# Optimization experiments

Hardware: AMD Instinct MI355X
Metric: run time of the kernel (lower is better)

Reference implementation:

```python
import jax, jax.numpy as jnp
import numpy as np

C = 64          # channels / d_model
D_INNER = 128   # expand * C
D_STATE = 16
D_CONV = 4
DT_RANK = 4     # ceil(C / 16)
GROUPS = 4
EPS = 1e-5


def setup_inputs() -> dict:
    key = jax.random.key(0)
    ks = jax.random.split(key, 12)
    b, h, w = 2, 128, 128
    s = 0.02
    return {
        "x": jax.random.normal(ks[0], (b, C, h, w), jnp.float32),
        "in_proj_w": jax.random.normal(ks[1], (2 * D_INNER, C), jnp.float32) * s,
        "conv_w": jax.random.normal(ks[2], (D_INNER, D_CONV), jnp.float32) * s,
        "conv_b": jnp.zeros((D_INNER,), jnp.float32),
        "x_proj_w": jax.random.normal(ks[3], (DT_RANK + 2 * D_STATE, D_INNER), jnp.float32) * s,
        "dt_proj_w": jax.random.normal(ks[4], (D_INNER, DT_RANK), jnp.float32) * s,
        "dt_proj_b": jax.random.normal(ks[5], (D_INNER,), jnp.float32) * s,
        "A_log": jnp.log(jnp.broadcast_to(jnp.arange(1, D_STATE + 1, dtype=jnp.float32), (D_INNER, D_STATE))),
        "D": jnp.ones((D_INNER,), jnp.float32),
        "out_proj_w": jax.random.normal(ks[6], (C, D_INNER), jnp.float32) * s,
        "gn_scale": jnp.ones((C,), jnp.float32),
        "gn_bias": jnp.zeros((C,), jnp.float32),
    }


def _mamba(xr, in_proj_w, conv_w, conv_b, x_proj_w, dt_proj_w, dt_proj_b, A_log, D, out_proj_w):
    # xr: (b, L, C)
    b, L, _ = xr.shape
    xz = jnp.einsum('blc,ec->ble', xr, in_proj_w)          # (b, L, 2*d_inner)
    xc, z = jnp.split(xz, 2, axis=-1)
    # causal depthwise conv1d, kernel D_CONV
    xp = jnp.pad(xc, ((0, 0), (D_CONV - 1, 0), (0, 0)))
    xconv = sum(conv_w[:, k] * xp[:, k:k + L, :] for k in range(D_CONV)) + conv_b
    u = jax.nn.silu(xconv)                                  # (b, L, d_inner)
    dbc = jnp.einsum('bld,ed->ble', u, x_proj_w)
    dt_r = dbc[..., :DT_RANK]
    Bm = dbc[..., DT_RANK:DT_RANK + D_STATE]                # (b, L, d_state)
    Cm = dbc[..., DT_RANK + D_STATE:]                       # (b, L, d_state)
    dt = jax.nn.softplus(jnp.einsum('blr,dr->bld', dt_r, dt_proj_w) + dt_proj_b)
    A = -jnp.exp(A_log)                                     # (d_inner, d_state)
    deltaA = jnp.exp(dt[..., None] * A)                     # (b, L, d_inner, d_state)
    deltaBu = (dt * u)[..., None] * Bm[:, :, None, :]       # (b, L, d_inner, d_state)

    def step(hst, inp):
        dA_t, dBu_t, C_t = inp
        hst = dA_t * hst + dBu_t                            # (b, d_inner, d_state)
        y_t = jnp.einsum('bds,bs->bd', hst, C_t)
        return hst, y_t

    h0 = jnp.zeros((b, D_INNER, D_STATE), xr.dtype)
    _, ys = jax.lax.scan(step, h0, (jnp.moveaxis(deltaA, 1, 0), jnp.moveaxis(deltaBu, 1, 0), jnp.moveaxis(Cm, 1, 0)))
    y = jnp.moveaxis(ys, 0, 1) + u * D                      # (b, L, d_inner)
    y = y * jax.nn.silu(z)
    return jnp.einsum('bld,cd->blc', y, out_proj_w)


def _group_norm_silu(x, scale, bias):
    # x: (b, C, h, w)
    b, c, h, w = x.shape
    xg = x.reshape(b, GROUPS, c // GROUPS, h, w)
    mu = xg.mean(axis=(2, 3, 4), keepdims=True)
    var = xg.var(axis=(2, 3, 4), keepdims=True)
    xn = ((xg - mu) * jax.lax.rsqrt(var + EPS)).reshape(b, c, h, w)
    return jax.nn.silu(xn * scale[None, :, None, None] + bias[None, :, None, None])


def reference(x, in_proj_w, conv_w, conv_b, x_proj_w, dt_proj_w, dt_proj_b, A_log, D, out_proj_w, gn_scale, gn_bias):
    b, c, h, w = x.shape
    xr = jnp.transpose(x, (0, 2, 3, 1)).reshape(b, h * w, c)
    y = _mamba(xr, in_proj_w, conv_w, conv_b, x_proj_w, dt_proj_w, dt_proj_b, A_log, D, out_proj_w)
    y = jnp.transpose(y.reshape(b, h, w, c), (0, 3, 1, 2))
    y = _group_norm_silu(y, gn_scale, gn_bias)
    return y + x
```

## Files before the change

kernel.cpp:

```cpp
#include <hip/hip_runtime.h>

#define BB 2
#define CCH 64
#define LLEN 16384
#define DM 128
#define NCHK 512
#define TCHK 32
#define NGRP 32
#define JG 16
#define NG 4

#define OFF_XC   0ull
#define OFF_HEND 0ull
#define OFF_HLOC 2097152ull
#define OFF_Z    4194304ull
#define OFF_U    8388608ull
#define OFF_DT   12582912ull
#define OFF_BM   16777216ull
#define OFF_CM   17301504ull
#define OFF_DTS  17825792ull
#define OFF_YM   17956864ull
#define OFF_WC   17956864ull
#define OFF_STAT 20054016ull
#define OFF_CUMDT 20971520ull
#define OFF_GEND  21102592ull
#define OFF_GDT   21233664ull
#define OFF_GINIT 21241856ull

__device__ __forceinline__ float fsilu(float v) {
  return v * __builtin_amdgcn_rcpf(1.f + __expf(-v));
}
__device__ __forceinline__ float fsoftplus(float v) {
  return v > 20.f ? v : __logf(1.f + __expf(v));
}

__global__ __launch_bounds__(256) void k1_inproj(
    const float* __restrict__ x, const float* __restrict__ w,
    float* __restrict__ xc, float* __restrict__ z)
{
  const int b = blockIdx.z;
  const int l0 = blockIdx.x * 64;
  const int e0 = blockIdx.y * 64;
  __shared__ float As[64][68];
  __shared__ float Bs[64][68];
  const int t = threadIdx.x;
#pragma unroll
  for (int i = 0; i < 4; i++) {
    int f4 = t + i * 256;
    int c = f4 >> 4, tok4 = (f4 & 15) * 4;
    *reinterpret_cast<float4*>(&As[c][tok4]) =
        *reinterpret_cast<const float4*>(&x[(size_t)(b * CCH + c) * LLEN + l0 + tok4]);
  }
#pragma unroll
  for (int i = 0; i < 16; i++) {
    int idx = t + i * 256;
    int e = idx >> 6, c = idx & 63;
    Bs[c][e] = w[(e0 + e) * CCH + c];
  }
  __syncthreads();
  const int tm = (t & 15) * 4;
  const int tn = (t >> 4) * 4;
  float acc[4][4] = {};
  for (int c = 0; c < 64; c++) {
    float4 av = *reinterpret_cast<const float4*>(&As[c][tm]);
    float4 bv = *reinterpret_cast<const float4*>(&Bs[c][tn]);
    acc[0][0] += av.x * bv.x; acc[0][1] += av.x * bv.y; acc[0][2] += av.x * bv.z; acc[0][3] += av.x * bv.w;
    acc[1][0] += av.y * bv.x; acc[1][1] += av.y * bv.y; acc[1][2] += av.y * bv.z; acc[1][3] += av.y * bv.w;
    acc[2][0] += av.z * bv.x; acc[2][1] += av.z * bv.y; acc[2][2] += av.z * bv.z; acc[2][3] += av.z * bv.w;
    acc[3][0] += av.w * bv.x; acc[3][1] += av.w * bv.y; acc[3][2] += av.w * bv.z; acc[3][3] += av.w * bv.w;
  }
  float* dst = (e0 < DM) ? (xc + e0) : (z + (e0 - DM));
#pragma unroll
  for (int i = 0; i < 4; i++) {
    int l = l0 + tm + i;
    float4 v = make_float4(acc[i][0], acc[i][1], acc[i][2], acc[i][3]);
    *reinterpret_cast<float4*>(dst + (size_t)(b * LLEN + l) * DM + tn) = v;
  }
}

__global__ __launch_bounds__(256) void k0_wcomb(
    const float* __restrict__ xpw, const float* __restrict__ dtw, float* __restrict__ wc,
    float* __restrict__ stat)
{
  int i = blockIdx.x * 256 + threadIdx.x;
  if (blockIdx.x == 0 && threadIdx.x < BB * NG * 2) stat[threadIdx.x] = 0.f;
  if (i >= 160 * 128) return;
  int e = i >> 7, dd = i & 127;
  float v;
  if (e < 128) {
    v = dtw[e * 4 + 0] * xpw[0 * 128 + dd] + dtw[e * 4 + 1] * xpw[1 * 128 + dd]
      + dtw[e * 4 + 2] * xpw[2 * 128 + dd] + dtw[e * 4 + 3] * xpw[3 * 128 + dd];
  } else {
    v = xpw[(e - 128 + 4) * 128 + dd];
  }
  wc[i] = v;
}

__global__ __launch_bounds__(256) void k2a_conv(
    const float* __restrict__ xc, const float* __restrict__ cw, const float* __restrict__ cb,
    float* __restrict__ u)
{
  const int t = threadIdx.x;
  const int d4 = (t & 31) * 4;
  const int tg = t >> 5;
  const int tok0 = blockIdx.x * 64 + tg * 8;
  const int l0 = tok0 & (LLEN - 1);
  float4 w0 = *reinterpret_cast<const float4*>(cw + (d4 + 0) * 4);
  float4 w1 = *reinterpret_cast<const float4*>(cw + (d4 + 1) * 4);
  float4 w2 = *reinterpret_cast<const float4*>(cw + (d4 + 2) * 4);
  float4 w3 = *reinterpret_cast<const float4*>(cw + (d4 + 3) * 4);
  float4 bias = *reinterpret_cast<const float4*>(cb + d4);
  float4 row[11];
#pragma unroll
  for (int r = 0; r < 11; r++) {
    int l = l0 - 3 + r;
    if (l < 0) row[r] = make_float4(0.f, 0.f, 0.f, 0.f);
    else row[r] = *reinterpret_cast<const float4*>(xc + (size_t)(tok0 - 3 + r) * DM + d4);
  }
#pragma unroll
  for (int j = 0; j < 8; j++) {
    float4 acc;
    acc.x = bias.x + w0.x * row[j].x + w0.y * row[j+1].x + w0.z * row[j+2].x + w0.w * row[j+3].x;
    acc.y = bias.y + w1.x * row[j].y + w1.y * row[j+1].y + w1.z * row[j+2].y + w1.w * row[j+3].y;
    acc.z = bias.z + w2.x * row[j].z + w2.y * row[j+1].z + w2.z * row[j+2].z + w2.w * row[j+3].z;
    acc.w = bias.w + w3.x * row[j].w + w3.y * row[j+1].w + w3.z * row[j+2].w + w3.w * row[j+3].w;
    acc.x = fsilu(acc.x); acc.y = fsilu(acc.y); acc.z = fsilu(acc.z); acc.w = fsilu(acc.w);
    *reinterpret_cast<float4*>(u + (size_t)(tok0 + j) * DM + d4) = acc;
  }
}

__global__ __launch_bounds__(128) void k2b_proj(
    const float* __restrict__ u, const float* __restrict__ wc, const float* __restrict__ dtpb,
    float* __restrict__ dt, float* __restrict__ bm, float* __restrict__ cm)
{
  const int tok0 = blockIdx.x * 64;
  const int e0 = blockIdx.y * 32;
  const int t = threadIdx.x;
  __shared__ float As[64][68];
  __shared__ float Bs[64][36];
  const int tm = (t & 15) * 4;
  const int tn = (t >> 4) * 4;
  float acc[4][4] = {};
  for (int kb = 0; kb < 2; kb++) {
#pragma unroll
    for (int i2 = 0; i2 < 2; i2++) {
      int tile = t + i2 * 128;
      int kt4 = (tile & 15) * 4, tok4 = (tile >> 4) * 4;
      const float* gp = u + (size_t)(tok0 + tok4) * DM + kb * 64 + kt4;
      float4 r0 = *reinterpret_cast<const float4*>(gp + 0 * DM);
      float4 r1 = *reinterpret_cast<const float4*>(gp + 1 * DM);
      float4 r2 = *reinterpret_cast<const float4*>(gp + 2 * DM);
      float4 r3 = *reinterpret_cast<const float4*>(gp + 3 * DM);
      *reinterpret_cast<float4*>(&As[kt4 + 0][tok4]) = make_float4(r0.x, r1.x, r2.x, r3.x);
      *reinterpret_cast<float4*>(&As[kt4 + 1][tok4]) = make_float4(r0.y, r1.y, r2.y, r3.y);
      *reinterpret_cast<float4*>(&As[kt4 + 2][tok4]) = make_float4(r0.z, r1.z, r2.z, r3.z);
      *reinterpret_cast<float4*>(&As[kt4 + 3][tok4]) = make_float4(r0.w, r1.w, r2.w, r3.w);
    }
    {
      int kt4 = (t & 15) * 4, et4 = (t >> 4) * 4;
      const float* gp = wc + (size_t)(e0 + et4) * DM + kb * 64 + kt4;
      float4 r0 = *reinterpret_cast<const float4*>(gp + 0 * DM);
      float4 r1 = *reinterpret_cast<const float4*>(gp + 1 * DM);
      float4 r2 = *reinterpret_cast<const float4*>(gp + 2 * DM);
      float4 r3 = *reinterpret_cast<const float4*>(gp + 3 * DM);
      *reinterpret_cast<float4*>(&Bs[kt4 + 0][et4]) = make_float4(r0.x, r1.x, r2.x, r3.x);
      *reinterpret_cast<float4*>(&Bs[kt4 + 1][et4]) = make_float4(r0.y, r1.y, r2.y, r3.y);
      *reinterpret_cast<float4*>(&Bs[kt4 + 2][et4]) = make_float4(r0.z, r1.z, r2.z, r3.z);
      *reinterpret_cast<float4*>(&Bs[kt4 + 3][et4]) = make_float4(r0.w, r1.w, r2.w, r3.w);
    }
    __syncthreads();
#pragma unroll 4
    for (int k = 0; k < 64; k++) {
      float4 av = *reinterpret_cast<const float4*>(&As[k][tm]);
      float4 bv = *reinterpret_cast<const float4*>(&Bs[k][tn]);
      acc[0][0] += av.x * bv.x; acc[0][1] += av.x * bv.y; acc[0][2] += av.x * bv.z; acc[0][3] += av.x * bv.w;
      acc[1][0] += av.y * bv.x; acc[1][1] += av.y * bv.y; acc[1][2] += av.y * bv.z; acc[1][3] += av.y * bv.w;
      acc[2][0] += av.z * bv.x; acc[2][1] += av.z * bv.y; acc[2][2] += av.z * bv.z; acc[2][3] += av.z * bv.w;
      acc[3][0] += av.w * bv.x; acc[3][1] += av.w * bv.y; acc[3][2] += av.w * bv.z; acc[3][3] += av.w * bv.w;
    }
    __syncthreads();
  }
  float* Cs = &As[0][0];
#pragma unroll
  for (int i = 0; i < 4; i++) {
#pragma unroll
    for (int j = 0; j < 4; j++) Cs[(tm + i) * 33 + tn + j] = acc[i][j];
  }
  __syncthreads();
  if (e0 < DM) {
#pragma unroll
    for (int i = 0; i < 16; i++) {
      int idx = t + i * 128;
      int tok = idx >> 5, e = idx & 31;
      float v = fsoftplus(Cs[tok * 33 + e] + dtpb[e0 + e]);
      dt[(size_t)(tok0 + tok) * DM + e0 + e] = v;
    }
  } else {
#pragma unroll
    for (int i = 0; i < 16; i++) {
      int idx = t + i * 128;
      int tok = idx >> 5, e = idx & 31;
      float v = Cs[tok * 33 + e];
      if (e < 16) bm[(size_t)(tok0 + tok) * 16 + e] = v;
      else        cm[(size_t)(tok0 + tok) * 16 + (e - 16)] = v;
    }
  }
}

__global__ __launch_bounds__(128) void k3_scan1(
    const float* __restrict__ dt, const float* __restrict__ u, const float* __restrict__ bm,
    const float* __restrict__ alog, float* __restrict__ hend, float* __restrict__ dts)
{
  const int b = blockIdx.y, ch = blockIdx.x;
  const int d = threadIdx.x;
  __shared__ float sb[TCHK][16];
  const size_t tok0 = (size_t)b * LLEN + (size_t)ch * TCHK;
  reinterpret_cast<float4*>(&sb[0][0])[d] = reinterpret_cast<const float4*>(bm + tok0 * 16)[d];
  float A[16];
  {
    const float4* ap = reinterpret_cast<const float4*>(alog + d * 16);
#pragma unroll
    for (int q = 0; q < 4; q++) {
      float4 v = ap[q];
      A[q * 4 + 0] = -__expf(v.x); A[q * 4 + 1] = -__expf(v.y);
      A[q * 4 + 2] = -__expf(v.z); A[q * 4 + 3] = -__expf(v.w);
    }
  }
  __syncthreads();
  float h[16];
#pragma unroll
  for (int s = 0; s < 16; s++) h[s] = 0.f;
  float dsum = 0.f;
  const float* dtp = dt + tok0 * DM + d;
  const float* up  = u  + tok0 * DM + d;
  for (int i = 0; i < TCHK; i++) {
    float dtv = dtp[(size_t)i * DM];
    float uv  = up[(size_t)i * DM];
    float dtu = dtv * uv;
    dsum += dtv;
    float bv[16];
#pragma unroll
    for (int q = 0; q < 4; q++)
      *reinterpret_cast<float4*>(&bv[q * 4]) = *reinterpret_cast<const float4*>(&sb[i][q * 4]);
#pragma unroll
    for (int s = 0; s < 16; s++) {
      float da = __expf(dtv * A[s]);
      h[s] = da * h[s] + dtu * bv[s];
    }
  }
  float* hp = hend + ((size_t)(b * DM + d) * NCHK + ch) * 16;
#pragma unroll
  for (int q = 0; q < 4; q++)
    reinterpret_cast<float4*>(hp)[q] = make_float4(h[q*4], h[q*4+1], h[q*4+2], h[q*4+3]);
  dts[(size_t)(b * DM + d) * NCHK + ch] = dsum;
}

__global__ __launch_bounds__(256) void k4a_group(
    const float* __restrict__ alog, const float* __restrict__ dts, const float* __restrict__ hend,
    float* __restrict__ hlocal, float* __restrict__ cumdt,
    float* __restrict__ gend, float* __restrict__ gdt)
{
  const int tid = blockIdx.x * 256 + threadIdx.x;
  const int s = tid & 15;
  const int bdg = tid >> 4;
  const int g = bdg & (NGRP - 1);
  const int bd = bdg >> 5;
  const int d = bd & (DM - 1);
  const float A = -__expf(alog[d * 16 + s]);
  const int ch0 = g * JG;
  const float* hp = hend + ((size_t)bd * NCHK + ch0) * 16 + s;
  const float* dp = dts + (size_t)bd * NCHK + ch0;
  float* hl = hlocal + ((size_t)bd * NCHK + ch0) * 16 + s;
  float hb[JG], db[JG];
#pragma unroll
  for (int j = 0; j < JG; j++) { hb[j] = hp[j * 16]; db[j] = dp[j]; }
  float h = 0.f, cd = 0.f;
#pragma unroll
  for (int j = 0; j < JG; j++) {
    hl[j * 16] = h;
    if (s == 0) cumdt[(size_t)(ch0 + j) * (BB * DM) + bd] = cd;
    h = __expf(A * db[j]) * h + hb[j];
    cd += db[j];
  }
  gend[(size_t)bdg * 16 + s] = h;
  if (s == 0) gdt[bdg] = cd;
}

__global__ __launch_bounds__(64) void k4b_combine(
    const float* __restrict__ alog, const float* __restrict__ gdt, const float* __restrict__ gend,
    float* __restrict__ ginit)
{
  const int tid = blockIdx.x * 64 + threadIdx.x;
  const int s = tid & 15, bd = tid >> 4, d = bd & (DM - 1);
  const float A = -__expf(alog[d * 16 + s]);
  const float* ge = gend + (size_t)bd * NGRP * 16 + s;
  const float* gd = gdt + (size_t)bd * NGRP;
  float* gi = ginit + (size_t)bd * NGRP * 16 + s;
  float gb[NGRP], db[NGRP];
#pragma unroll
  for (int g = 0; g < NGRP; g++) { gb[g] = ge[g * 16]; db[g] = gd[g]; }
  float h = 0.f;
#pragma unroll
  for (int g = 0; g < NGRP; g++) {
    gi[g * 16] = h;
    h = __expf(A * db[g]) * h + gb[g];
  }
}

__global__ __launch_bounds__(256) void k5f_scan_out(
    const float* __restrict__ dt, const float* __restrict__ u, const float* __restrict__ bm,
    const float* __restrict__ cm, const float* __restrict__ alog, const float* __restrict__ Dv,
    const float* __restrict__ z, const float* __restrict__ hlocal,
    const float* __restrict__ cumdt, const float* __restrict__ ginit,
    const float* __restrict__ ow, float* __restrict__ ym, float* __restrict__ stat)
{
  const int b = blockIdx.y, bx = blockIdx.x;
  const int t = threadIdx.x;
  const int ch2 = t >> 7;
  const int d = t & 127;
  const int ch = bx * 2 + ch2;
  __shared__ float sb[2][TCHK][16];
  __shared__ float sc[2][TCHK][16];
  __shared__ float Ys[DM][72];
  __shared__ float Bs[DM][68];
  const size_t tokb = (size_t)b * LLEN + (size_t)bx * 64;
  const size_t tok0 = tokb + (size_t)ch2 * TCHK;
  reinterpret_cast<float4*>(&sb[0][0][0])[t] = reinterpret_cast<const float4*>(bm + tokb * 16)[t];
  reinterpret_cast<float4*>(&sc[0][0][0])[t] = reinterpret_cast<const float4*>(cm + tokb * 16)[t];
#pragma unroll
  for (int i2 = 0; i2 < 2; i2++) {
    int tile = t + i2 * 256;
    int c4 = (tile & 15) * 4;
    int dl4 = (tile >> 4) * 4;
    const float* gp = ow + (size_t)c4 * DM + dl4;
    float4 r0 = *reinterpret_cast<const float4*>(gp + 0 * DM);
    float4 r1 = *reinterpret_cast<const float4*>(gp + 1 * DM);
    float4 r2 = *reinterpret_cast<const float4*>(gp + 2 * DM);
    float4 r3 = *reinterpret_cast<const float4*>(gp + 3 * DM);
    *reinterpret_cast<float4*>(&Bs[dl4 + 0][c4]) = make_float4(r0.x, r1.x, r2.x, r3.x);
    *reinterpret_cast<float4*>(&Bs[dl4 + 1][c4]) = make_float4(r0.y, r1.y, r2.y, r3.y);
    *reinterpret_cast<float4*>(&Bs[dl4 + 2][c4]) = make_float4(r0.z, r1.z, r2.z, r3.z);
    *reinterpret_cast<float4*>(&Bs[dl4 + 3][c4]) = make_float4(r0.w, r1.w, r2.w, r3.w);
  }
  float A[16];
  {
    const float4* ap = reinterpret_cast<const float4*>(alog + d * 16);
#pragma unroll
    for (int q = 0; q < 4; q++) {
      float4 v = ap[q];
      A[q * 4 + 0] = -__expf(v.x); A[q * 4 + 1] = -__expf(v.y);
      A[q * 4 + 2] = -__expf(v.z); A[q * 4 + 3] = -__expf(v.w);
    }
  }
  const float Dd = Dv[d];
  const int bd = b * DM + d;
  const int g = ch / JG;
  const float cd = cumdt[(size_t)ch * (BB * DM) + bd];
  float h[16];
  {
    const float4* hlp = reinterpret_cast<const float4*>(hlocal + ((size_t)bd * NCHK + ch) * 16);
    const float4* gip = reinterpret_cast<const float4*>(ginit + ((size_t)(bd * NGRP + g)) * 16);
#pragma unroll
    for (int q = 0; q < 4; q++) {
      float4 hl = hlp[q];
      float4 gi = gip[q];
      h[q * 4 + 0] = __expf(A[q * 4 + 0] * cd) * gi.x + hl.x;
      h[q * 4 + 1] = __expf(A[q * 4 + 1] * cd) * gi.y + hl.y;
      h[q * 4 + 2] = __expf(A[q * 4 + 2] * cd) * gi.z + hl.z;
      h[q * 4 + 3] = __expf(A[q * 4 + 3] * cd) * gi.w + hl.w;
    }
  }
  __syncthreads();
  const float* dtp = dt + tok0 * DM + d;
  const float* up = u + tok0 * DM + d;
  const float* zp = z + tok0 * DM + d;
  for (int i = 0; i < TCHK; i++) {
    float dtv = dtp[(size_t)i * DM];
    float uv  = up[(size_t)i * DM];
    float zv  = zp[(size_t)i * DM];
    float dtu = dtv * uv;
    float bv[16], cv[16];
#pragma unroll
    for (int q = 0; q < 4; q++) {
      *reinterpret_cast<float4*>(&bv[q * 4]) = *reinterpret_cast<const float4*>(&sb[ch2][i][q * 4]);
      *reinterpret_cast<float4*>(&cv[q * 4]) = *reinterpret_cast<const float4*>(&sc[ch2][i][q * 4]);
    }
    float y = 0.f;
#pragma unroll
    for (int s = 0; s < 16; s++) {
      float da = __expf(dtv * A[s]);
      h[s] = da * h[s] + dtu * bv[s];
      y += h[s] * cv[s];
    }
    Ys[d][ch2 * TCHK + i] = (y + uv * Dd) * fsilu(zv);
  }
  __syncthreads();
  const int tm = (t & 15) * 4;
  const int tn = (t >> 4) * 4;
  float acc[4][4] = {};
  for (int k = 0; k < DM; k++) {
    float4 av = *reinterpret_cast<const float4*>(&Ys[k][tm]);
    float4 bv = *reinterpret_cast<const float4*>(&Bs[k][tn]);
    acc[0][0] += av.x * bv.x; acc[0][1] += av.x * bv.y; acc[0][2] += av.x * bv.z; acc[0][3] += av.x * bv.w;
    acc[1][0] += av.y * bv.x; acc[1][1] += av.y * bv.y; acc[1][2] += av.y * bv.z; acc[1][3] += av.y * bv.w;
    acc[2][0] += av.z * bv.x; acc[2][1] += av.z * bv.y; acc[2][2] += av.z * bv.z; acc[2][3] += av.z * bv.w;
    acc[3][0] += av.w * bv.x; acc[3][1] += av.w * bv.y; acc[3][2] += av.w * bv.z; acc[3][3] += av.w * bv.w;
  }
  float lsum = 0.f, lssq = 0.f;
#pragma unroll
  for (int i = 0; i < 4; i++) {
    float4 v = make_float4(acc[i][0], acc[i][1], acc[i][2], acc[i][3]);
    *reinterpret_cast<float4*>(ym + (tokb + tm + i) * 64 + tn) = v;
    lsum += v.x + v.y + v.z + v.w;
    lssq += v.x * v.x + v.y * v.y + v.z * v.z + v.w * v.w;
  }
  __shared__ float sg[NG * 2];
  if (t < NG * 2) sg[t] = 0.f;
  __syncthreads();
  const int gg = tn >> 4;
  atomicAdd(&sg[gg * 2 + 0], lsum);
  atomicAdd(&sg[gg * 2 + 1], lssq);
  __syncthreads();
  if (t < NG * 2) atomicAdd(&stat[b * NG * 2 + t], sg[t]);
}

__global__ __launch_bounds__(256) void k7_gn(
    const float* __restrict__ ym, const float* __restrict__ stat,
    const float* __restrict__ scale, const float* __restrict__ bias,
    const float* __restrict__ x, float* __restrict__ out)
{
  const int b = blockIdx.y;
  const int p0 = blockIdx.x * 64;
  const int t = threadIdx.x;
  __shared__ float Ts[64][65];
#pragma unroll
  for (int i = 0; i < 16; i++) {
    int idx = t + i * 256;
    int p = idx >> 6, c = idx & 63;
    Ts[c][p] = ym[(size_t)(b * LLEN + p0 + p) * 64 + c];
  }
  __syncthreads();
  const float invN = 1.f / (16.f * 16384.f);
#pragma unroll
  for (int i = 0; i < 16; i++) {
    int idx = t + i * 256;
    int c = idx >> 6, p = idx & 63;
    int g = c >> 4;
    float mu = stat[b * 8 + g * 2] * invN;
    float var = stat[b * 8 + g * 2 + 1] * invN - mu * mu;
    float rs = rsqrtf(var + 1e-5f);
    float v = (Ts[c][p] - mu) * rs * scale[c] + bias[c];
    size_t o = (size_t)(b * CCH + c) * LLEN + p0 + p;
    out[o] = fsilu(v) + x[o];
  }
}

extern "C" void kernel_launch(void* const* d_in, const int* in_sizes, int n_in,
                              void* d_out, int out_size, void* d_ws, size_t ws_size,
                              hipStream_t stream)
{
  const float* x    = (const float*)d_in[0];
  const float* ipw  = (const float*)d_in[1];
  const float* cw   = (const float*)d_in[2];
  const float* cb   = (const float*)d_in[3];
  const float* xpw  = (const float*)d_in[4];
  const float* dtw  = (const float*)d_in[5];
  const float* dtpb = (const float*)d_in[6];
  const float* alog = (const float*)d_in[7];
  const float* Dv   = (const float*)d_in[8];
  const float* ow   = (const float*)d_in[9];
  const float* gns  = (const float*)d_in[10];
  const float* gnb  = (const float*)d_in[11];

  float* ws    = (float*)d_ws;
  float* xc    = ws + OFF_XC;
  float* hend  = ws + OFF_HEND;
  float* hloc  = ws + OFF_HLOC;
  float* z     = ws + OFF_Z;
  float* u     = ws + OFF_U;
  float* dt    = ws + OFF_DT;
  float* bm    = ws + OFF_BM;
  float* cm    = ws + OFF_CM;
  float* dts   = ws + OFF_DTS;
  float* ym    = ws + OFF_YM;
  float* wc    = ws + OFF_WC;
  float* cumdt = ws + OFF_CUMDT;
  float* gend  = ws + OFF_GEND;
  float* gdt   = ws + OFF_GDT;
  float* ginit = ws + OFF_GINIT;
  float* stat  = ws + OFF_STAT;
  float* out   = (float*)d_out;

  k0_wcomb<<<dim3(80), 256, 0, stream>>>(xpw, dtw, wc, stat);
  k1_inproj<<<dim3(LLEN / 64, 4, BB), 256, 0, stream>>>(x, ipw, xc, z);
  k2a_conv<<<dim3(BB * LLEN / 64), 256, 0, stream>>>(xc, cw, cb, u);
  k2b_proj<<<dim3(BB * LLEN / 64, 5), 128, 0, stream>>>(u, wc, dtpb, dt, bm, cm);
  k3_scan1<<<dim3(NCHK, BB), 128, 0, stream>>>(dt, u, bm, alog, hend, dts);
  k4a_group<<<dim3(BB * DM * NGRP * 16 / 256), 256, 0, stream>>>(alog, dts, hend, hloc, cumdt, gend, gdt);
  k4b_combine<<<dim3(BB * DM * 16 / 64), 64, 0, stream>>>(alog, gdt, gend, ginit);
  k5f_scan_out<<<dim3(NCHK / 2, BB), 256, 0, stream>>>(dt, u, bm, cm, alog, Dv, z, hloc, cumdt, ginit, ow, ym, stat);
  k7_gn<<<dim3(LLEN / 64, BB), 256, 0, stream>>>(ym, stat, gns, gnb, x, out);
}
```

Baseline: 133.4 us.

## Split scan state across thread pairs, fold weight-combine kernel into in-proj, use exp2

Both scan kernels now give each (channel, chunk) two threads that each hold half of the 16 SSM states. The output kernel combines their partial y with a lane shuffle and runs the out-projection with 512 threads on smaller tiles. This doubles the number of threads working on the latency-bound serial recurrences, and exponentials switch to exp2 with a log2e-prescaled A. The separate weight-combine/stat-zero kernel is merged into block (0,0,0) of the in-proj kernel to save a launch. That one block now does extra serial work, and the per-thread dt/u loads are duplicated across each thread pair.

```diff
diff --git a/kernel.cpp b/kernel.cpp
--- a/kernel.cpp
+++ b/kernel.cpp
@@ -9,6 +9,7 @@
 #define NGRP 32
 #define JG 16
 #define NG 4
+#define LOG2E 1.44269504f
 
 #define OFF_XC   0ull
 #define OFF_HEND 0ull
@@ -36,14 +37,30 @@
 
 __global__ __launch_bounds__(256) void k1_inproj(
     const float* __restrict__ x, const float* __restrict__ w,
-    float* __restrict__ xc, float* __restrict__ z)
+    float* __restrict__ xc, float* __restrict__ z,
+    const float* __restrict__ xpw, const float* __restrict__ dtw,
+    float* __restrict__ wc, float* __restrict__ stat)
 {
   const int b = blockIdx.z;
   const int l0 = blockIdx.x * 64;
   const int e0 = blockIdx.y * 64;
+  const int t = threadIdx.x;
+  if (blockIdx.x == 0 && blockIdx.y == 0 && blockIdx.z == 0) {
+    if (t < BB * NG * 2) stat[t] = 0.f;
+    for (int i = t; i < 160 * 128; i += 256) {
+      int e = i >> 7, dd = i & 127;
+      float v;
+      if (e < 128) {
+        v = dtw[e * 4 + 0] * xpw[0 * 128 + dd] + dtw[e * 4 + 1] * xpw[1 * 128 + dd]
+          + dtw[e * 4 + 2] * xpw[2 * 128 + dd] + dtw[e * 4 + 3] * xpw[3 * 128 + dd];
+      } else {
+        v = xpw[(e - 128 + 4) * 128 + dd];
+      }
+      wc[i] = v;
+    }
+  }
   __shared__ float As[64][68];
   __shared__ float Bs[64][68];
-  const int t = threadIdx.x;
 #pragma unroll
   for (int i = 0; i < 4; i++) {
     int f4 = t + i * 256;
@@ -76,24 +93,6 @@
     float4 v = make_float4(acc[i][0], acc[i][1], acc[i][2], acc[i][3]);
     *reinterpret_cast<float4*>(dst + (size_t)(b * LLEN + l) * DM + tn) = v;
   }
-}
-
-__global__ __launch_bounds__(256) void k0_wcomb(
-    const float* __restrict__ xpw, const float* __restrict__ dtw, float* __restrict__ wc,
-    float* __restrict__ stat)
-{
-  int i = blockIdx.x * 256 + threadIdx.x;
-  if (blockIdx.x == 0 && threadIdx.x < BB * NG * 2) stat[threadIdx.x] = 0.f;
-  if (i >= 160 * 128) return;
-  int e = i >> 7, dd = i & 127;
-  float v;
-  if (e < 128) {
-    v = dtw[e * 4 + 0] * xpw[0 * 128 + dd] + dtw[e * 4 + 1] * xpw[1 * 128 + dd]
-      + dtw[e * 4 + 2] * xpw[2 * 128 + dd] + dtw[e * 4 + 3] * xpw[3 * 128 + dd];
-  } else {
-    v = xpw[(e - 128 + 4) * 128 + dd];
-  }
-  wc[i] = v;
 }
 
 __global__ __launch_bounds__(256) void k2a_conv(
@@ -207,29 +206,32 @@
   }
 }
 
-__global__ __launch_bounds__(128) void k3_scan1(
+__global__ __launch_bounds__(256) void k3_scan1(
     const float* __restrict__ dt, const float* __restrict__ u, const float* __restrict__ bm,
     const float* __restrict__ alog, float* __restrict__ hend, float* __restrict__ dts)
 {
   const int b = blockIdx.y, ch = blockIdx.x;
-  const int d = threadIdx.x;
+  const int t = threadIdx.x;
+  const int sh = t & 1;
+  const int d = t >> 1;
   __shared__ float sb[TCHK][16];
   const size_t tok0 = (size_t)b * LLEN + (size_t)ch * TCHK;
-  reinterpret_cast<float4*>(&sb[0][0])[d] = reinterpret_cast<const float4*>(bm + tok0 * 16)[d];
-  float A[16];
+  if (t < 128)
+    reinterpret_cast<float4*>(&sb[0][0])[t] = reinterpret_cast<const float4*>(bm + tok0 * 16)[t];
+  float A2[8];
   {
-    const float4* ap = reinterpret_cast<const float4*>(alog + d * 16);
-#pragma unroll
-    for (int q = 0; q < 4; q++) {
+    const float4* ap = reinterpret_cast<const float4*>(alog + d * 16 + sh * 8);
+#pragma unroll
+    for (int q = 0; q < 2; q++) {
       float4 v = ap[q];
-      A[q * 4 + 0] = -__expf(v.x); A[q * 4 + 1] = -__expf(v.y);
-      A[q * 4 + 2] = -__expf(v.z); A[q * 4 + 3] = -__expf(v.w);
-    }
-  }
-  __syncthreads();
-  float h[16];
-#pragma unroll
-  for (int s = 0; s < 16; s++) h[s] = 0.f;
+      A2[q * 4 + 0] = -__expf(v.x) * LOG2E; A2[q * 4 + 1] = -__expf(v.y) * LOG2E;
+      A2[q * 4 + 2] = -__expf(v.z) * LOG2E; A2[q * 4 + 3] = -__expf(v.w) * LOG2E;
+    }
+  }
+  __syncthreads();
+  float h[8];
+#pragma unroll
+  for (int s = 0; s < 8; s++) h[s] = 0.f;
   float dsum = 0.f;
   const float* dtp = dt + tok0 * DM + d;
   const float* up  = u  + tok0 * DM + d;
@@ -238,21 +240,21 @@
     float uv  = up[(size_t)i * DM];
     float dtu = dtv * uv;
     dsum += dtv;
-    float bv[16];
-#pragma unroll
-    for (int q = 0; q < 4; q++)
-      *reinterpret_cast<float4*>(&bv[q * 4]) = *reinterpret_cast<const float4*>(&sb[i][q * 4]);
-#pragma unroll
-    for (int s = 0; s < 16; s++) {
-      float da = __expf(dtv * A[s]);
+    float bv[8];
+#pragma unroll
+    for (int q = 0; q < 2; q++)
+      *reinterpret_cast<float4*>(&bv[q * 4]) = *reinterpret_cast<const float4*>(&sb[i][sh * 8 + q * 4]);
+#pragma unroll
+    for (int s = 0; s < 8; s++) {
+      float da = exp2f(dtv * A2[s]);
       h[s] = da * h[s] + dtu * bv[s];
     }
   }
-  float* hp = hend + ((size_t)(b * DM + d) * NCHK + ch) * 16;
-#pragma unroll
-  for (int q = 0; q < 4; q++)
+  float* hp = hend + ((size_t)(b * DM + d) * NCHK + ch) * 16 + sh * 8;
+#pragma unroll
+  for (int q = 0; q < 2; q++)
     reinterpret_cast<float4*>(hp)[q] = make_float4(h[q*4], h[q*4+1], h[q*4+2], h[q*4+3]);
-  dts[(size_t)(b * DM + d) * NCHK + ch] = dsum;
+  if (sh == 0) dts[(size_t)(b * DM + d) * NCHK + ch] = dsum;
 }
 
 __global__ __launch_bounds__(256) void k4a_group(
@@ -307,7 +309,7 @@
   }
 }
 
-__global__ __launch_bounds__(256) void k5f_scan_out(
+__global__ __launch_bounds__(512) void k5f_scan_out(
     const float* __restrict__ dt, const float* __restrict__ u, const float* __restrict__ bm,
     const float* __restrict__ cm, const float* __restrict__ alog, const float* __restrict__ Dv,
     const float* __restrict__ z, const float* __restrict__ hlocal,
@@ -316,22 +318,23 @@
 {
   const int b = blockIdx.y, bx = blockIdx.x;
   const int t = threadIdx.x;
-  const int ch2 = t >> 7;
-  const int d = t & 127;
+  const int sh = t & 1;
+  const int d = (t >> 1) & 127;
+  const int ch2 = t >> 8;
   const int ch = bx * 2 + ch2;
   __shared__ float sb[2][TCHK][16];
   __shared__ float sc[2][TCHK][16];
-  __shared__ float Ys[DM][72];
+  __shared__ float Ys[DM][66];
   __shared__ float Bs[DM][68];
   const size_t tokb = (size_t)b * LLEN + (size_t)bx * 64;
   const size_t tok0 = tokb + (size_t)ch2 * TCHK;
-  reinterpret_cast<float4*>(&sb[0][0][0])[t] = reinterpret_cast<const float4*>(bm + tokb * 16)[t];
-  reinterpret_cast<float4*>(&sc[0][0][0])[t] = reinterpret_cast<const float4*>(cm + tokb * 16)[t];
-#pragma unroll
-  for (int i2 = 0; i2 < 2; i2++) {
-    int tile = t + i2 * 256;
-    int c4 = (tile & 15) * 4;
-    int dl4 = (tile >> 4) * 4;
+  if (t < 256) {
+    reinterpret_cast<float4*>(&sb[0][0][0])[t] = reinterpret_cast<const float4*>(bm + tokb * 16)[t];
+    reinterpret_cast<float4*>(&sc[0][0][0])[t] = reinterpret_cast<const float4*>(cm + tokb * 16)[t];
+  }
+  {
+    int c4 = (t & 15) * 4;
+    int dl4 = (t >> 4) * 4;
     const float* gp = ow + (size_t)c4 * DM + dl4;
     float4 r0 = *reinterpret_cast<const float4*>(gp + 0 * DM);
     float4 r1 = *reinterpret_cast<const float4*>(gp + 1 * DM);
@@ -342,32 +345,32 @@
     *reinterpret_cast<float4*>(&Bs[dl4 + 2][c4]) = make_float4(r0.z, r1.z, r2.z, r3.z);
     *reinterpret_cast<float4*>(&Bs[dl4 + 3][c4]) = make_float4(r0.w, r1.w, r2.w, r3.w);
   }
-  float A[16];
+  float A2[8];
   {
-    const float4* ap = reinterpret_cast<const float4*>(alog + d * 16);
-#pragma unroll
-    for (int q = 0; q < 4; q++) {
+    const float4* ap = reinterpret_cast<const float4*>(alog + d * 16 + sh * 8);
+#pragma unroll
+    for (int q = 0; q < 2; q++) {
       float4 v = ap[q];
-      A[q * 4 + 0] = -__expf(v.x); A[q * 4 + 1] = -__expf(v.y);
-      A[q * 4 + 2] = -__expf(v.z); A[q * 4 + 3] = -__expf(v.w);
+      A2[q * 4 + 0] = -__expf(v.x) * LOG2E; A2[q * 4 + 1] = -__expf(v.y) * LOG2E;
+      A2[q * 4 + 2] = -__expf(v.z) * LOG2E; A2[q * 4 + 3] = -__expf(v.w) * LOG2E;
     }
   }
   const float Dd = Dv[d];
   const int bd = b * DM + d;
   const int g = ch / JG;
   const float cd = cumdt[(size_t)ch * (BB * DM) + bd];
-  float h[16];
+  float h[8];
   {
-    const float4* hlp = reinterpret_cast<const float4*>(hlocal + ((size_t)bd * NCHK + ch) * 16);
-    const float4* gip = reinterpret_cast<const float4*>(ginit + ((size_t)(bd * NGRP + g)) * 16);
-#pragma unroll
-    for (int q = 0; q < 4; q++) {
+    const float4* hlp = reinterpret_cast<const float4*>(hlocal + ((size_t)bd * NCHK + ch) * 16 + sh * 8);
+    const float4* gip = reinterpret_cast<const float4*>(ginit + ((size_t)(bd * NGRP + g)) * 16 + sh * 8);
+#pragma unroll
+    for (int q = 0; q < 2; q++) {
       float4 hl = hlp[q];
       float4 gi = gip[q];
-      h[q * 4 + 0] = __expf(A[q * 4 + 0] * cd) * gi.x + hl.x;
-      h[q * 4 + 1] = __expf(A[q * 4 + 1] * cd) * gi.y + hl.y;
-      h[q * 4 + 2] = __expf(A[q * 4 + 2] * cd) * gi.z + hl.z;
-      h[q * 4 + 3] = __expf(A[q * 4 + 3] * cd) * gi.w + hl.w;
+      h[q * 4 + 0] = exp2f(A2[q * 4 + 0] * cd) * gi.x + hl.x;
+      h[q * 4 + 1] = exp2f(A2[q * 4 + 1] * cd) * gi.y + hl.y;
+      h[q * 4 + 2] = exp2f(A2[q * 4 + 2] * cd) * gi.z + hl.z;
+      h[q * 4 + 3] = exp2f(A2[q * 4 + 3] * cd) * gi.w + hl.w;
     }
   }
   __syncthreads();
@@ -379,45 +382,44 @@
     float uv  = up[(size_t)i * DM];
     float zv  = zp[(size_t)i * DM];
     float dtu = dtv * uv;
-    float bv[16], cv[16];
-#pragma unroll
-    for (int q = 0; q < 4; q++) {
-      *reinterpret_cast<float4*>(&bv[q * 4]) = *reinterpret_cast<const float4*>(&sb[ch2][i][q * 4]);
-      *reinterpret_cast<float4*>(&cv[q * 4]) = *reinterpret_cast<const float4*>(&sc[ch2][i][q * 4]);
+    float bv[8], cv[8];
+#pragma unroll
+    for (int q = 0; q < 2; q++) {
+      *reinterpret_cast<float4*>(&bv[q * 4]) = *reinterpret_cast<const float4*>(&sb[ch2][i][sh * 8 + q * 4]);
+      *reinterpret_cast<float4*>(&cv[q * 4]) = *reinterpret_cast<const float4*>(&sc[ch2][i][sh * 8 + q * 4]);
     }
     float y = 0.f;
 #pragma unroll
-    for (int s = 0; s < 16; s++) {
-      float da = __expf(dtv * A[s]);
+    for (int s = 0; s < 8; s++) {
+      float da = exp2f(dtv * A2[s]);
       h[s] = da * h[s] + dtu * bv[s];
       y += h[s] * cv[s];
     }
-    Ys[d][ch2 * TCHK + i] = (y + uv * Dd) * fsilu(zv);
-  }
-  __syncthreads();
-  const int tm = (t & 15) * 4;
-  const int tn = (t >> 4) * 4;
-  float acc[4][4] = {};
+    y += __shfl_xor(y, 1);
+    if (sh == 0) Ys[d][ch2 * TCHK + i] = (y + uv * Dd) * fsilu(zv);
+  }
+  __syncthreads();
+  const int tm2 = (t & 31) * 2;
+  const int tn4 = (t >> 5) * 4;
+  float acc[2][4] = {};
   for (int k = 0; k < DM; k++) {
-    float4 av = *reinterpret_cast<const float4*>(&Ys[k][tm]);
-    float4 bv = *reinterpret_cast<const float4*>(&Bs[k][tn]);
+    float2 av = *reinterpret_cast<const float2*>(&Ys[k][tm2]);
+    float4 bv = *reinterpret_cast<const float4*>(&Bs[k][tn4]);
     acc[0][0] += av.x * bv.x; acc[0][1] += av.x * bv.y; acc[0][2] += av.x * bv.z; acc[0][3] += av.x * bv.w;
     acc[1][0] += av.y * bv.x; acc[1][1] += av.y * bv.y; acc[1][2] += av.y * bv.z; acc[1][3] += av.y * bv.w;
-    acc[2][0] += av.z * bv.x; acc[2][1] += av.z * bv.y; acc[2][2] += av.z * bv.z; acc[2][3] += av.z * bv.w;
-    acc[3][0] += av.w * bv.x; acc[3][1] += av.w * bv.y; acc[3][2] += av.w * bv.z; acc[3][3] += av.w * bv.w;
   }
   float lsum = 0.f, lssq = 0.f;
 #pragma unroll
-  for (int i = 0; i < 4; i++) {
+  for (int i = 0; i < 2; i++) {
     float4 v = make_float4(acc[i][0], acc[i][1], acc[i][2], acc[i][3]);
-    *reinterpret_cast<float4*>(ym + (tokb + tm + i) * 64 + tn) = v;
+    *reinterpret_cast<float4*>(ym + (tokb + tm2 + i) * 64 + tn4) = v;
     lsum += v.x + v.y + v.z + v.w;
     lssq += v.x * v.x + v.y * v.y + v.z * v.z + v.w * v.w;
   }
   __shared__ float sg[NG * 2];
   if (t < NG * 2) sg[t] = 0.f;
   __syncthreads();
-  const int gg = tn >> 4;
+  const int gg = tn4 >> 4;
   atomicAdd(&sg[gg * 2 + 0], lsum);
   atomicAdd(&sg[gg * 2 + 1], lssq);
   __syncthreads();
@@ -491,13 +493,12 @@
   float* stat  = ws + OFF_STAT;
   float* out   = (float*)d_out;
 
-  k0_wcomb<<<dim3(80), 256, 0, stream>>>(xpw, dtw, wc, stat);
-  k1_inproj<<<dim3(LLEN / 64, 4, BB), 256, 0, stream>>>(x, ipw, xc, z);
+  k1_inproj<<<dim3(LLEN / 64, 4, BB), 256, 0, stream>>>(x, ipw, xc, z, xpw, dtw, wc, stat);
   k2a_conv<<<dim3(BB * LLEN / 64), 256, 0, stream>>>(xc, cw, cb, u);
   k2b_proj<<<dim3(BB * LLEN / 64, 5), 128, 0, stream>>>(u, wc, dtpb, dt, bm, cm);
-  k3_scan1<<<dim3(NCHK, BB), 128, 0, stream>>>(dt, u, bm, alog, hend, dts);
+  k3_scan1<<<dim3(NCHK, BB), 256, 0, stream>>>(dt, u, bm, alog, hend, dts);
   k4a_group<<<dim3(BB * DM * NGRP * 16 / 256), 256, 0, stream>>>(alog, dts, hend, hloc, cumdt, gend, gdt);
   k4b_combine<<<dim3(BB * DM * 16 / 64), 64, 0, stream>>>(alog, gdt, gend, ginit);
-  k5f_scan_out<<<dim3(NCHK / 2, BB), 256, 0, stream>>>(dt, u, bm, cm, alog, Dv, z, hloc, cumdt, ginit, ow, ym, stat);
+  k5f_scan_out<<<dim3(NCHK / 2, BB), 512, 0, stream>>>(dt, u, bm, cm, alog, Dv, z, hloc, cumdt, ginit, ow, ym, stat);
   k7_gn<<<dim3(LLEN / 64, BB), 256, 0, stream>>>(ym, stat, gns, gnb, x, out);
 }
```

Result: slower. 152.5 us (+14.3%).
